# Optimization experiments

Hardware: AMD Instinct MI355X
Metric: run time of the kernel (lower is better)

Reference implementation:

```python
import jax, jax.numpy as jnp
import numpy as np

IN, OUT, HID = 64, 32, 256
B, T = 64, 256
NOISE_STD, TAU = 0.05, 0.2


def setup_inputs() -> dict:
    key = jax.random.key(0)
    ks = jax.random.split(key, 8)
    u = jax.random.normal(ks[0], (B, T, IN), dtype=jnp.float32)
    x0 = jax.random.normal(ks[1], (B, HID), dtype=jnp.float32)
    noise = jax.random.normal(ks[2], (T, B, HID), dtype=jnp.float32)
    w_hh_rnn = jax.random.normal(ks[3], (HID, HID), dtype=jnp.float32) * (0.1 / HID ** 0.5)
    w_hh_tbrnn = jax.random.normal(ks[4], (HID, HID, HID), dtype=jnp.float32) * (0.1 / HID)
    w_in_w = jax.random.normal(ks[5], (HID, IN), dtype=jnp.float32)
    w_in_b = jnp.zeros((HID,), dtype=jnp.float32)
    w_out_w = jax.random.normal(ks[6], (OUT, HID), dtype=jnp.float32) * 4.0
    w_out_b = jax.random.normal(ks[7], (OUT,), dtype=jnp.float32) * 0.0
    return {"u": u, "x0": x0, "noise": noise, "w_hh_rnn": w_hh_rnn,
            "w_hh_tbrnn": w_hh_tbrnn, "w_in_w": w_in_w, "w_in_b": w_in_b,
            "w_out_w": w_out_w, "w_out_b": w_out_b}


def reference(u, x0, noise, w_hh_rnn, w_hh_tbrnn, w_in_w, w_in_b, w_out_w, w_out_b):
    # mode='cont', form='rate', adv=False, nonlinearity=tanh, output_nonlinearity=tanh
    u_t_first = jnp.transpose(u, (1, 0, 2))  # [T, B, IN]

    def step(x, inp):
        u_t, n_t = inp
        r = jnp.tanh(x)                                   # rate form
        input_I = u_t @ w_in_w.T + w_in_b                 # [B, HID]
        hidden_W1 = r @ w_hh_rnn.T                        # [B, HID]
        # out[b,j] = sum_{i,k} r[b,i] * W[j,i,k] * r[b,k]
        hidden_W2 = jnp.einsum('bi,jik,bk->bj', r, w_hh_tbrnn, r)
        rec_x = hidden_W1 + hidden_W2 + input_I
        x_new = x + NOISE_STD * n_t + TAU * (-x + rec_x)  # cont mode
        return x_new, x_new

    x_final, traj = jax.lax.scan(step, x0, (u_t_first, noise))
    trajectories = jnp.transpose(traj, (1, 0, 2))         # [B, T, HID]
    output = jnp.tanh(trajectories) @ w_out_w.T + w_out_b  # [B, T, OUT]
    return output, x_final, trajectories
```

## Files before the change

### kernel.cpp

```cpp
#include <hip/hip_runtime.h>
#include <hip/hip_bf16.h>
#include <math.h>

#define HID 256
#define BSZ 64
#define TLEN 256
#define INW 64
#define OUTW 32
#define NOISE_STD 0.05f
#define TAU 0.2f

typedef __attribute__((ext_vector_type(8))) short short8;
typedef __attribute__((ext_vector_type(4))) short shortx4;
typedef __attribute__((ext_vector_type(4))) float floatx4;
typedef unsigned long long u64;

__device__ __forceinline__ int ridx(int b, int k) {
    int P = ((b >> 2) & 7) ^ ((b & 3) << 1);
    return b * 256 + ((((k >> 3) ^ P) & 31) << 3) + (k & 7);
}

__global__ __launch_bounds__(256) void swizzle_kernel(const float* __restrict__ W,
                                                      __hip_bfloat16* __restrict__ Wsw) {
    int g = blockIdx.x * 256 + threadIdx.x;
    int l  = g & 63;
    int ni = (g >> 6) & 15;
    int kk = (g >> 10) & 7;
    int j  = g >> 13;
    int i  = ni * 16 + (l & 15);
    int k0 = kk * 32 + (l >> 4) * 8;
    const float* __restrict__ src = W + ((size_t)j * HID + i) * HID + k0;
    __hip_bfloat16* __restrict__ dst = Wsw + (size_t)g * 8;
#pragma unroll
    for (int e = 0; e < 8; ++e) dst[e] = __float2bfloat16(src[e]);
}

__global__ __launch_bounds__(256) void init_kernel(const float* __restrict__ x0,
                                                   u64* __restrict__ buf0) {
    int g = blockIdx.x;
    int k = threadIdx.x;
    u64 v = 0;
#pragma unroll
    for (int e = 0; e < 4; ++e) {
        __hip_bfloat16 h = __float2bfloat16(tanhf(x0[(4 * g + e) * HID + k]));
        v |= (u64)(*(unsigned short*)&h) << (16 * e);
    }
    buf0[g * 256 + k] = v;
}

__global__ __launch_bounds__(256) void pre_kernel(const float* __restrict__ u,
                                                  const float* __restrict__ w_in_w,
                                                  const float* __restrict__ w_in_b,
                                                  const float* __restrict__ noise,
                                                  float* __restrict__ pre) {
    __shared__ float ulds[BSZ][INW + 4];
    const int t = blockIdx.x;
    const int j = threadIdx.x;
    {
        int b = threadIdx.x >> 2, q = threadIdx.x & 3;
#pragma unroll
        for (int e = 0; e < 4; ++e) {
            float4 v = *(const float4*)(u + ((size_t)b * TLEN + t) * INW + q * 16 + e * 4);
            *(float4*)&ulds[b][q * 16 + e * 4] = v;
        }
    }
    float wreg[INW];
#pragma unroll
    for (int q = 0; q < INW / 4; ++q) {
        float4 v = *(const float4*)(w_in_w + (size_t)j * INW + q * 4);
        wreg[q * 4 + 0] = v.x; wreg[q * 4 + 1] = v.y;
        wreg[q * 4 + 2] = v.z; wreg[q * 4 + 3] = v.w;
    }
    float bias = w_in_b[j];
    __syncthreads();
    for (int b = 0; b < BSZ; ++b) {
        float s = bias;
#pragma unroll
        for (int in_ = 0; in_ < INW; ++in_) s = fmaf(ulds[b][in_], wreg[in_], s);
        float nz = noise[((size_t)t * BSZ + b) * HID + j];
        pre[((size_t)t * HID + j) * BSZ + b] = NOISE_STD * nz + TAU * s;
    }
}

__global__ __launch_bounds__(256, 1) void persist_kernel(
    const __hip_bfloat16* __restrict__ Wsw,
    const float* __restrict__ w_hh,
    const float* __restrict__ u,
    const float* __restrict__ w_in_w,
    const float* __restrict__ w_in_b,
    const float* __restrict__ noise,
    const float* __restrict__ x0,
    u64* __restrict__ buf0,
    u64* __restrict__ buf1,
    float* __restrict__ traj,
    float* __restrict__ trajWS,
    float* __restrict__ xfinal,
    int* __restrict__ ready,
    const float* __restrict__ pre,
    int use_pre, int use_tws) {
    __shared__ short rlds[16384];
    __shared__ float redw[256];
    __shared__ char lds_pad[57344];

    const int tid  = threadIdx.x;
    const int j    = blockIdx.x;
    const int w    = tid >> 6;
    const int lane = tid & 63;
    const int quad = lane >> 4;
    const int col  = lane & 15;

    if (j == 0x7fffffff) lds_pad[tid] = 0;

    short8 wreg[32];
    {
        const short* __restrict__ wsh = (const short*)Wsw;
#pragma unroll
        for (int kk = 0; kk < 8; ++kk)
#pragma unroll
            for (int mt = 0; mt < 4; ++mt)
                wreg[kk * 4 + mt] = *(const short8*)(wsh +
                    ((((size_t)j * 8 + kk) * 16 + (w * 4 + mt)) * 64 + lane) * 8);
    }
    float whh16[16];
#pragma unroll
    for (int mt = 0; mt < 4; ++mt)
#pragma unroll
        for (int rg = 0; rg < 4; ++rg)
            whh16[mt * 4 + rg] = w_hh[j * HID + (w * 4 + mt) * 16 + quad * 4 + rg];

    float xb = 0.f;
    if (tid < BSZ) xb = x0[tid * HID + j];

#pragma unroll 1
    for (int t = 0; t < TLEN; ++t) {
        const u64* __restrict__ rcur = (t & 1) ? buf1 : buf0;
        u64* __restrict__ rnxt = (t & 1) ? buf0 : buf1;

        float extra = 0.f;
        if (tid < BSZ) {
            if (use_pre) {
                extra = pre[((size_t)t * HID + j) * BSZ + tid];
            } else {
                float isum = w_in_b[j];
                const float4* __restrict__ urow =
                    (const float4*)(u + ((size_t)tid * TLEN + t) * INW);
                const float4* __restrict__ wrow = (const float4*)(w_in_w + (size_t)j * INW);
#pragma unroll
                for (int q = 0; q < INW / 4; ++q) {
                    float4 uu = urow[q], ww = wrow[q];
                    isum = fmaf(uu.x, ww.x, isum);
                    isum = fmaf(uu.y, ww.y, isum);
                    isum = fmaf(uu.z, ww.z, isum);
                    isum = fmaf(uu.w, ww.w, isum);
                }
                float nz = noise[((size_t)t * BSZ + tid) * HID + j];
                extra = NOISE_STD * nz + TAU * isum;
            }
        }

        if (t > 0) {
            while (__hip_atomic_load(ready + tid * 16, __ATOMIC_RELAXED,
                                     __HIP_MEMORY_SCOPE_AGENT) < t)
                __builtin_amdgcn_s_sleep(1);
            asm volatile("" ::: "memory");
        }

        {
            u64 v[16];
#pragma unroll
            for (int g = 0; g < 16; ++g)
                v[g] = __hip_atomic_load(rcur + g * 256 + tid, __ATOMIC_RELAXED,
                                         __HIP_MEMORY_SCOPE_AGENT);
#pragma unroll
            for (int g = 0; g < 16; ++g)
#pragma unroll
                for (int e = 0; e < 4; ++e)
                    rlds[ridx(4 * g + e, tid)] = (short)(v[g] >> (16 * e));
        }
        __syncthreads();

        floatx4 acc[4][4];
#pragma unroll
        for (int mt = 0; mt < 4; ++mt)
#pragma unroll
            for (int nt = 0; nt < 4; ++nt) acc[mt][nt] = (floatx4){0.f, 0.f, 0.f, 0.f};

#pragma unroll
        for (int kk = 0; kk < 8; ++kk) {
            short8 afrag[4];
#pragma unroll
            for (int nt = 0; nt < 4; ++nt)
                afrag[nt] = *(const short8*)&rlds[ridx(nt * 16 + col, kk * 32 + quad * 8)];
#pragma unroll
            for (int mt = 0; mt < 4; ++mt)
#pragma unroll
                for (int nt = 0; nt < 4; ++nt)
                    acc[mt][nt] = __builtin_amdgcn_mfma_f32_16x16x32_bf16(
                        wreg[kk * 4 + mt], afrag[nt], acc[mt][nt], 0, 0, 0);
        }

        float part[4];
#pragma unroll
        for (int nt = 0; nt < 4; ++nt) part[nt] = 0.f;
#pragma unroll
        for (int mt = 0; mt < 4; ++mt) {
            const int ib = (w * 4 + mt) * 16 + quad * 4;
#pragma unroll
            for (int nt = 0; nt < 4; ++nt) {
                const int b = nt * 16 + col;
                shortx4 r4 = *(const shortx4*)&rlds[ridx(b, ib)];
#pragma unroll
                for (int rg = 0; rg < 4; ++rg) {
                    short rs = r4[rg];
                    float rv = __bfloat162float(*(__hip_bfloat16*)&rs);
                    part[nt] = fmaf(rv, acc[mt][nt][rg] + whh16[mt * 4 + rg], part[nt]);
                }
            }
        }
#pragma unroll
        for (int nt = 0; nt < 4; ++nt) {
            part[nt] += __shfl_xor(part[nt], 16, 64);
            part[nt] += __shfl_xor(part[nt], 32, 64);
        }
        if (quad == 0) {
#pragma unroll
            for (int nt = 0; nt < 4; ++nt)
                redw[w * 64 + nt * 16 + col] = part[nt];
        }
        __syncthreads();

        if (w == 0) {
            const int b = lane;
            float rec = redw[b] + redw[64 + b] + redw[128 + b] + redw[192 + b];
            float xn = xb + extra + TAU * (rec - xb);
            xb = xn;

            if (t < TLEN - 1) {
                __hip_bfloat16 h = __float2bfloat16(tanhf(xn));
                int hs = (int)(*(unsigned short*)&h);
                int src = 4 * (lane & 15);
                u64 pv = (u64)(unsigned)__shfl(hs, src + 0, 64)
                       | ((u64)(unsigned)__shfl(hs, src + 1, 64) << 16)
                       | ((u64)(unsigned)__shfl(hs, src + 2, 64) << 32)
                       | ((u64)(unsigned)__shfl(hs, src + 3, 64) << 48);
                if (lane < 16)
                    __hip_atomic_store(rnxt + (size_t)lane * 256 + j, pv,
                                       __ATOMIC_RELAXED, __HIP_MEMORY_SCOPE_AGENT);
                asm volatile("s_waitcnt vmcnt(0)" ::: "memory");
                if (lane == 0)
                    __hip_atomic_store(ready + j * 16, t + 1, __ATOMIC_RELAXED,
                                       __HIP_MEMORY_SCOPE_AGENT);
            }

            if (use_tws) {
                trajWS[((size_t)t * HID + j) * BSZ + b] = xn;
            } else {
                traj[((size_t)b * TLEN + t) * HID + j] = xn;
                if (t == TLEN - 1) xfinal[b * HID + j] = xn;
            }
        }
    }
}

__global__ __launch_bounds__(256) void fixup_kernel(
    const float* __restrict__ trajWS,
    const float* __restrict__ w_out_w,
    const float* __restrict__ w_out_b,
    float* __restrict__ traj,
    float* __restrict__ xfinal,
    float* __restrict__ out) {
    __shared__ float xv[BSZ * 257];
    __shared__ float wol[OUTW * 257];
    const int t = blockIdx.x, tid = threadIdx.x;

#pragma unroll
    for (int it = 0; it < 16; ++it) {
        int flat = it * 1024 + tid * 4;
        float4 v = *(const float4*)(trajWS + (size_t)t * 16384 + flat);
        int jj = flat >> 6, b = flat & 63;
        xv[(b + 0) * 257 + jj] = v.x;
        xv[(b + 1) * 257 + jj] = v.y;
        xv[(b + 2) * 257 + jj] = v.z;
        xv[(b + 3) * 257 + jj] = v.w;
    }
#pragma unroll
    for (int it = 0; it < 8; ++it) {
        int flat = it * 1024 + tid * 4;
        float4 v = *(const float4*)(w_out_w + flat);
        int o = flat >> 8, h = flat & 255;
        *(float4*)&wol[o * 257 + h] = v;
    }
    __syncthreads();

    for (int b = 0; b < BSZ; ++b)
        traj[((size_t)b * TLEN + t) * HID + tid] = xv[b * 257 + tid];
    if (t == TLEN - 1)
        for (int b = 0; b < BSZ; ++b)
            xfinal[b * HID + tid] = xv[b * 257 + tid];

    __syncthreads();
#pragma unroll
    for (int it = 0; it < 64; ++it)
        xv[it * 257 + tid] = tanhf(xv[it * 257 + tid]);
    __syncthreads();

    const int o = tid & 31;
    const float bias = w_out_b[o];
#pragma unroll 1
    for (int rep = 0; rep < 8; ++rep) {
        int b = rep * 8 + (tid >> 5);
        float s = bias;
#pragma unroll 8
        for (int h = 0; h < HID; ++h)
            s = fmaf(xv[b * 257 + h], wol[o * 257 + h], s);
        out[((size_t)b * TLEN + t) * OUTW + o] = s;
    }
}

__global__ __launch_bounds__(256) void output_kernel(
    const float* __restrict__ traj, const float* __restrict__ w_out_w,
    const float* __restrict__ w_out_b, float* __restrict__ out) {
    __shared__ float th[8][HID + 1];
    const int bt0 = blockIdx.x * 8;
    const int tid = threadIdx.x;
#pragma unroll
    for (int m = 0; m < 8; ++m) {
        int idx = m * 256 + tid;
        th[idx >> 8][idx & 255] = tanhf(traj[(size_t)bt0 * HID + idx]);
    }
    __syncthreads();
    const int row = tid >> 5, o = tid & 31;
    const float* __restrict__ wrow = w_out_w + (size_t)o * HID;
    float s = w_out_b[o];
#pragma unroll 8
    for (int h = 0; h < HID; ++h) s = fmaf(th[row][h], wrow[h], s);
    out[(size_t)(bt0 + row) * OUTW + o] = s;
}

extern "C" void kernel_launch(void* const* d_in, const int* in_sizes, int n_in,
                              void* d_out, int out_size, void* d_ws, size_t ws_size,
                              hipStream_t stream) {
    const float* u       = (const float*)d_in[0];
    const float* x0      = (const float*)d_in[1];
    const float* noise   = (const float*)d_in[2];
    const float* w_hh    = (const float*)d_in[3];
    const float* W       = (const float*)d_in[4];
    const float* w_in_w  = (const float*)d_in[5];
    const float* w_in_b  = (const float*)d_in[6];
    const float* w_out_w = (const float*)d_in[7];
    const float* w_out_b = (const float*)d_in[8];

    float* out    = (float*)d_out;
    float* xfinal = out + (size_t)BSZ * TLEN * OUTW;
    float* traj   = xfinal + (size_t)BSZ * HID;

    char* ws = (char*)d_ws;
    __hip_bfloat16* Wsw = (__hip_bfloat16*)ws;
    u64*   buf0 = (u64*)(ws + 33554432);
    u64*   buf1 = (u64*)(ws + 33587200);
    int*   rdy  = (int*)(ws + 33619968);
    float* tws  = (float*)(ws + 33636352);
    float* pre  = (float*)(ws + 50413568);
    const size_t NEED_TWS = 50413568ull;
    const size_t NEED_PRE = 67190784ull;
    const int use_tws = (ws_size >= NEED_TWS) ? 1 : 0;
    const int use_pre = (ws_size >= NEED_PRE) ? 1 : 0;

    hipMemsetAsync(rdy, 0, 16384, stream);
    swizzle_kernel<<<8192, 256, 0, stream>>>(W, Wsw);
    init_kernel<<<16, 256, 0, stream>>>(x0, buf0);
    if (use_pre)
        pre_kernel<<<TLEN, 256, 0, stream>>>(u, w_in_w, w_in_b, noise, pre);

    persist_kernel<<<256, 256, 0, stream>>>(
        Wsw, w_hh, u, w_in_w, w_in_b, noise, x0,
        buf0, buf1, traj, tws, xfinal, rdy, pre, use_pre, use_tws);

    if (use_tws)
        fixup_kernel<<<TLEN, 256, 0, stream>>>(tws, w_out_w, w_out_b, traj, xfinal, out);
    else
        output_kernel<<<(BSZ * TLEN) / 8, 256, 0, stream>>>(traj, w_out_w, w_out_b, out);
}
```

Measured before the change: 1.471 ms.

## Split K across two wave groups in persistent recurrent kernel with 512 threads

```diff
diff --git a/kernel.cpp b/kernel.cpp
--- a/kernel.cpp
+++ b/kernel.cpp
@@ -82,7 +82,7 @@
     }
 }
 
-__global__ __launch_bounds__(256, 1) void persist_kernel(
+__global__ __launch_bounds__(512, 1) void persist_kernel(
     const __hip_bfloat16* __restrict__ Wsw,
     const float* __restrict__ w_hh,
     const float* __restrict__ u,
@@ -99,8 +99,7 @@
     const float* __restrict__ pre,
     int use_pre, int use_tws) {
     __shared__ short rlds[16384];
-    __shared__ float redw[256];
-    __shared__ char lds_pad[57344];
+    __shared__ float redw[512];
 
     const int tid  = threadIdx.x;
     const int j    = blockIdx.x;
@@ -108,25 +107,28 @@
     const int lane = tid & 63;
     const int quad = lane >> 4;
     const int col  = lane & 15;
-
-    if (j == 0x7fffffff) lds_pad[tid] = 0;
-
-    short8 wreg[32];
+    const int wk   = w >> 2;
+    const int wi   = w & 3;
+    const int kcol = tid & 255;
+    const int gb   = (tid >> 8) * 8;
+
+    short8 wreg[16];
     {
         const short* __restrict__ wsh = (const short*)Wsw;
 #pragma unroll
-        for (int kk = 0; kk < 8; ++kk)
+        for (int kkl = 0; kkl < 4; ++kkl)
 #pragma unroll
             for (int mt = 0; mt < 4; ++mt)
-                wreg[kk * 4 + mt] = *(const short8*)(wsh +
-                    ((((size_t)j * 8 + kk) * 16 + (w * 4 + mt)) * 64 + lane) * 8);
+                wreg[kkl * 4 + mt] = *(const short8*)(wsh +
+                    ((((size_t)j * 8 + (wk * 4 + kkl)) * 16 + (wi * 4 + mt)) * 64 + lane) * 8);
     }
     float whh16[16];
 #pragma unroll
     for (int mt = 0; mt < 4; ++mt)
 #pragma unroll
         for (int rg = 0; rg < 4; ++rg)
-            whh16[mt * 4 + rg] = w_hh[j * HID + (w * 4 + mt) * 16 + quad * 4 + rg];
+            whh16[mt * 4 + rg] = (wk == 0)
+                ? w_hh[j * HID + (wi * 4 + mt) * 16 + quad * 4 + rg] : 0.f;
 
     float xb = 0.f;
     if (tid < BSZ) xb = x0[tid * HID + j];
@@ -159,23 +161,23 @@
         }
 
         if (t > 0) {
-            while (__hip_atomic_load(ready + tid * 16, __ATOMIC_RELAXED,
+            while (__hip_atomic_load(ready + kcol * 16, __ATOMIC_RELAXED,
                                      __HIP_MEMORY_SCOPE_AGENT) < t)
                 __builtin_amdgcn_s_sleep(1);
             asm volatile("" ::: "memory");
         }
 
         {
-            u64 v[16];
-#pragma unroll
-            for (int g = 0; g < 16; ++g)
-                v[g] = __hip_atomic_load(rcur + g * 256 + tid, __ATOMIC_RELAXED,
-                                         __HIP_MEMORY_SCOPE_AGENT);
-#pragma unroll
-            for (int g = 0; g < 16; ++g)
+            u64 v[8];
+#pragma unroll
+            for (int gg = 0; gg < 8; ++gg)
+                v[gg] = __hip_atomic_load(rcur + (gb + gg) * 256 + kcol,
+                                          __ATOMIC_RELAXED, __HIP_MEMORY_SCOPE_AGENT);
+#pragma unroll
+            for (int gg = 0; gg < 8; ++gg)
 #pragma unroll
                 for (int e = 0; e < 4; ++e)
-                    rlds[ridx(4 * g + e, tid)] = (short)(v[g] >> (16 * e));
+                    rlds[ridx(4 * (gb + gg) + e, kcol)] = (short)(v[gg] >> (16 * e));
         }
         __syncthreads();
 
@@ -183,20 +185,23 @@
 #pragma unroll
         for (int mt = 0; mt < 4; ++mt)
 #pragma unroll
-            for (int nt = 0; nt < 4; ++nt) acc[mt][nt] = (floatx4){0.f, 0.f, 0.f, 0.f};
-
-#pragma unroll
-        for (int kk = 0; kk < 8; ++kk) {
+            for (int nt = 0; nt < 4; ++nt)
+                acc[mt][nt] = (floatx4){whh16[mt * 4 + 0], whh16[mt * 4 + 1],
+                                        whh16[mt * 4 + 2], whh16[mt * 4 + 3]};
+
+#pragma unroll
+        for (int kkl = 0; kkl < 4; ++kkl) {
             short8 afrag[4];
 #pragma unroll
             for (int nt = 0; nt < 4; ++nt)
-                afrag[nt] = *(const short8*)&rlds[ridx(nt * 16 + col, kk * 32 + quad * 8)];
+                afrag[nt] = *(const short8*)&rlds[
+                    ridx(nt * 16 + col, (wk * 4 + kkl) * 32 + quad * 8)];
 #pragma unroll
             for (int mt = 0; mt < 4; ++mt)
 #pragma unroll
                 for (int nt = 0; nt < 4; ++nt)
                     acc[mt][nt] = __builtin_amdgcn_mfma_f32_16x16x32_bf16(
-                        wreg[kk * 4 + mt], afrag[nt], acc[mt][nt], 0, 0, 0);
+                        wreg[kkl * 4 + mt], afrag[nt], acc[mt][nt], 0, 0, 0);
         }
 
         float part[4];
@@ -204,7 +209,7 @@
         for (int nt = 0; nt < 4; ++nt) part[nt] = 0.f;
 #pragma unroll
         for (int mt = 0; mt < 4; ++mt) {
-            const int ib = (w * 4 + mt) * 16 + quad * 4;
+            const int ib = (wi * 4 + mt) * 16 + quad * 4;
 #pragma unroll
             for (int nt = 0; nt < 4; ++nt) {
                 const int b = nt * 16 + col;
@@ -213,7 +218,7 @@
                 for (int rg = 0; rg < 4; ++rg) {
                     short rs = r4[rg];
                     float rv = __bfloat162float(*(__hip_bfloat16*)&rs);
-                    part[nt] = fmaf(rv, acc[mt][nt][rg] + whh16[mt * 4 + rg], part[nt]);
+                    part[nt] = fmaf(rv, acc[mt][nt][rg], part[nt]);
                 }
             }
         }
@@ -231,7 +236,9 @@
 
         if (w == 0) {
             const int b = lane;
-            float rec = redw[b] + redw[64 + b] + redw[128 + b] + redw[192 + b];
+            float rec = 0.f;
+#pragma unroll
+            for (int s = 0; s < 8; ++s) rec += redw[s * 64 + b];
             float xn = xb + extra + TAU * (rec - xb);
             xb = xn;
 
@@ -372,7 +379,7 @@
     if (use_pre)
         pre_kernel<<<TLEN, 256, 0, stream>>>(u, w_in_w, w_in_b, noise, pre);
 
-    persist_kernel<<<256, 256, 0, stream>>>(
+    persist_kernel<<<256, 512, 0, stream>>>(
         Wsw, w_hh, u, w_in_w, w_in_b, noise, x0,
         buf0, buf1, traj, tws, xfinal, rdy, pre, use_pre, use_tws);
 
```

After: 1.971 ms. +34.0%, slower.

## Replace double buffer with sentinel-marked triple ring to overlap state loads with flag wait

Applied to the files above, without the earlier changes.

```diff
diff --git a/kernel.cpp b/kernel.cpp
--- a/kernel.cpp
+++ b/kernel.cpp
@@ -9,6 +9,7 @@
 #define OUTW 32
 #define NOISE_STD 0.05f
 #define TAU 0.2f
+#define SENT 0xFFFFFFFFFFFFFFFFull
 
 typedef __attribute__((ext_vector_type(8))) short short8;
 typedef __attribute__((ext_vector_type(4))) short shortx4;
@@ -36,7 +37,7 @@
 }
 
 __global__ __launch_bounds__(256) void init_kernel(const float* __restrict__ x0,
-                                                   u64* __restrict__ buf0) {
+                                                   u64* __restrict__ ring0) {
     int g = blockIdx.x;
     int k = threadIdx.x;
     u64 v = 0;
@@ -45,7 +46,7 @@
         __hip_bfloat16 h = __float2bfloat16(tanhf(x0[(4 * g + e) * HID + k]));
         v |= (u64)(*(unsigned short*)&h) << (16 * e);
     }
-    buf0[g * 256 + k] = v;
+    ring0[g * 256 + k] = v;
 }
 
 __global__ __launch_bounds__(256) void pre_kernel(const float* __restrict__ u,
@@ -90,8 +91,7 @@
     const float* __restrict__ w_in_b,
     const float* __restrict__ noise,
     const float* __restrict__ x0,
-    u64* __restrict__ buf0,
-    u64* __restrict__ buf1,
+    u64* __restrict__ ring,
     float* __restrict__ traj,
     float* __restrict__ trajWS,
     float* __restrict__ xfinal,
@@ -133,8 +133,14 @@
 
 #pragma unroll 1
     for (int t = 0; t < TLEN; ++t) {
-        const u64* __restrict__ rcur = (t & 1) ? buf1 : buf0;
-        u64* __restrict__ rnxt = (t & 1) ? buf0 : buf1;
+        const u64* __restrict__ rslot = ring + (size_t)(t % 3) * 4096;
+        u64* __restrict__ wslot = ring + (size_t)((t + 1) % 3) * 4096;
+
+        u64 v[16];
+#pragma unroll
+        for (int g = 0; g < 16; ++g)
+            v[g] = __hip_atomic_load(rslot + g * 256 + tid, __ATOMIC_RELAXED,
+                                     __HIP_MEMORY_SCOPE_AGENT);
 
         float extra = 0.f;
         if (tid < BSZ) {
@@ -163,27 +169,38 @@
                                      __HIP_MEMORY_SCOPE_AGENT) < t)
                 __builtin_amdgcn_s_sleep(1);
             asm volatile("" ::: "memory");
-        }
-
-        {
-            u64 v[16];
-#pragma unroll
-            for (int g = 0; g < 16; ++g)
-                v[g] = __hip_atomic_load(rcur + g * 256 + tid, __ATOMIC_RELAXED,
-                                         __HIP_MEMORY_SCOPE_AGENT);
-#pragma unroll
-            for (int g = 0; g < 16; ++g)
-#pragma unroll
-                for (int e = 0; e < 4; ++e)
-                    rlds[ridx(4 * g + e, tid)] = (short)(v[g] >> (16 * e));
-        }
+            int pend = 1;
+            while (pend) {
+                pend = 0;
+#pragma unroll
+                for (int g = 0; g < 16; ++g)
+                    if (v[g] == SENT) {
+                        v[g] = __hip_atomic_load(rslot + g * 256 + tid,
+                                                 __ATOMIC_RELAXED,
+                                                 __HIP_MEMORY_SCOPE_AGENT);
+                        pend |= (v[g] == SENT);
+                    }
+            }
+        }
+
+#pragma unroll
+        for (int g = 0; g < 16; ++g)
+#pragma unroll
+            for (int e = 0; e < 4; ++e)
+                rlds[ridx(4 * g + e, tid)] = (short)(v[g] >> (16 * e));
         __syncthreads();
 
+        if (w == 0 && lane < 16)
+            __hip_atomic_store(ring + (size_t)((t + 2) % 3) * 4096 + lane * 256 + j,
+                               SENT, __ATOMIC_RELAXED, __HIP_MEMORY_SCOPE_AGENT);
+
         floatx4 acc[4][4];
 #pragma unroll
         for (int mt = 0; mt < 4; ++mt)
 #pragma unroll
-            for (int nt = 0; nt < 4; ++nt) acc[mt][nt] = (floatx4){0.f, 0.f, 0.f, 0.f};
+            for (int nt = 0; nt < 4; ++nt)
+                acc[mt][nt] = (floatx4){whh16[mt * 4 + 0], whh16[mt * 4 + 1],
+                                        whh16[mt * 4 + 2], whh16[mt * 4 + 3]};
 
 #pragma unroll
         for (int kk = 0; kk < 8; ++kk) {
@@ -213,7 +230,7 @@
                 for (int rg = 0; rg < 4; ++rg) {
                     short rs = r4[rg];
                     float rv = __bfloat162float(*(__hip_bfloat16*)&rs);
-                    part[nt] = fmaf(rv, acc[mt][nt][rg] + whh16[mt * 4 + rg], part[nt]);
+                    part[nt] = fmaf(rv, acc[mt][nt][rg], part[nt]);
                 }
             }
         }
@@ -244,7 +261,7 @@
                        | ((u64)(unsigned)__shfl(hs, src + 2, 64) << 32)
                        | ((u64)(unsigned)__shfl(hs, src + 3, 64) << 48);
                 if (lane < 16)
-                    __hip_atomic_store(rnxt + (size_t)lane * 256 + j, pv,
+                    __hip_atomic_store(wslot + (size_t)lane * 256 + j, pv,
                                        __ATOMIC_RELAXED, __HIP_MEMORY_SCOPE_AGENT);
                 asm volatile("s_waitcnt vmcnt(0)" ::: "memory");
                 if (lane == 0)
@@ -356,25 +373,25 @@
 
     char* ws = (char*)d_ws;
     __hip_bfloat16* Wsw = (__hip_bfloat16*)ws;
-    u64*   buf0 = (u64*)(ws + 33554432);
-    u64*   buf1 = (u64*)(ws + 33587200);
-    int*   rdy  = (int*)(ws + 33619968);
-    float* tws  = (float*)(ws + 33636352);
-    float* pre  = (float*)(ws + 50413568);
-    const size_t NEED_TWS = 50413568ull;
-    const size_t NEED_PRE = 67190784ull;
+    u64*   ring = (u64*)(ws + 33554432);
+    int*   rdy  = (int*)(ws + 33652736);
+    float* tws  = (float*)(ws + 33669120);
+    float* pre  = (float*)(ws + 50446336);
+    const size_t NEED_TWS = 50446336ull;
+    const size_t NEED_PRE = 67223552ull;
     const int use_tws = (ws_size >= NEED_TWS) ? 1 : 0;
     const int use_pre = (ws_size >= NEED_PRE) ? 1 : 0;
 
     hipMemsetAsync(rdy, 0, 16384, stream);
+    hipMemsetAsync((char*)ring + 32768, 0xFF, 65536, stream);
     swizzle_kernel<<<8192, 256, 0, stream>>>(W, Wsw);
-    init_kernel<<<16, 256, 0, stream>>>(x0, buf0);
+    init_kernel<<<16, 256, 0, stream>>>(x0, ring);
     if (use_pre)
         pre_kernel<<<TLEN, 256, 0, stream>>>(u, w_in_w, w_in_b, noise, pre);
 
     persist_kernel<<<256, 256, 0, stream>>>(
         Wsw, w_hh, u, w_in_w, w_in_b, noise, x0,
-        buf0, buf1, traj, tws, xfinal, rdy, pre, use_pre, use_tws);
+        ring, traj, tws, xfinal, rdy, pre, use_pre, use_tws);
 
     if (use_tws)
         fixup_kernel<<<TLEN, 256, 0, stream>>>(tws, w_out_w, w_out_b, traj, xfinal, out);
```

Result: slower. 3.120 ms (+112.0%).

## Split recurrent state fetch into halves and overlap second half with MFMA

Applied to the files above, without the earlier changes.

```diff
diff --git a/kernel.cpp b/kernel.cpp
--- a/kernel.cpp
+++ b/kernel.cpp
@@ -100,7 +100,6 @@
     int use_pre, int use_tws) {
     __shared__ short rlds[16384];
     __shared__ float redw[256];
-    __shared__ char lds_pad[57344];
 
     const int tid  = threadIdx.x;
     const int j    = blockIdx.x;
@@ -108,8 +107,9 @@
     const int lane = tid & 63;
     const int quad = lane >> 4;
     const int col  = lane & 15;
-
-    if (j == 0x7fffffff) lds_pad[tid] = 0;
+    const int kL   = tid & 127;
+    const int kH   = kL + 128;
+    const int gb   = (tid >> 7) * 8;
 
     short8 wreg[32];
     {
@@ -159,23 +159,22 @@
         }
 
         if (t > 0) {
-            while (__hip_atomic_load(ready + tid * 16, __ATOMIC_RELAXED,
+            while (__hip_atomic_load(ready + kL * 16, __ATOMIC_RELAXED,
                                      __HIP_MEMORY_SCOPE_AGENT) < t)
                 __builtin_amdgcn_s_sleep(1);
             asm volatile("" ::: "memory");
         }
-
         {
-            u64 v[16];
-#pragma unroll
-            for (int g = 0; g < 16; ++g)
-                v[g] = __hip_atomic_load(rcur + g * 256 + tid, __ATOMIC_RELAXED,
-                                         __HIP_MEMORY_SCOPE_AGENT);
-#pragma unroll
-            for (int g = 0; g < 16; ++g)
+            u64 vl[8];
+#pragma unroll
+            for (int gg = 0; gg < 8; ++gg)
+                vl[gg] = __hip_atomic_load(rcur + (gb + gg) * 256 + kL,
+                                           __ATOMIC_RELAXED, __HIP_MEMORY_SCOPE_AGENT);
+#pragma unroll
+            for (int gg = 0; gg < 8; ++gg)
 #pragma unroll
                 for (int e = 0; e < 4; ++e)
-                    rlds[ridx(4 * g + e, tid)] = (short)(v[g] >> (16 * e));
+                    rlds[ridx(4 * (gb + gg) + e, kL)] = (short)(vl[gg] >> (16 * e));
         }
         __syncthreads();
 
@@ -183,10 +182,17 @@
 #pragma unroll
         for (int mt = 0; mt < 4; ++mt)
 #pragma unroll
-            for (int nt = 0; nt < 4; ++nt) acc[mt][nt] = (floatx4){0.f, 0.f, 0.f, 0.f};
-
-#pragma unroll
-        for (int kk = 0; kk < 8; ++kk) {
+            for (int nt = 0; nt < 4; ++nt)
+                acc[mt][nt] = (floatx4){whh16[mt * 4 + 0], whh16[mt * 4 + 1],
+                                        whh16[mt * 4 + 2], whh16[mt * 4 + 3]};
+
+        int fh = t;
+        if (t > 0)
+            fh = __hip_atomic_load(ready + kH * 16, __ATOMIC_RELAXED,
+                                   __HIP_MEMORY_SCOPE_AGENT);
+
+#pragma unroll
+        for (int kk = 0; kk < 2; ++kk) {
             short8 afrag[4];
 #pragma unroll
             for (int nt = 0; nt < 4; ++nt)
@@ -199,6 +205,55 @@
                         wreg[kk * 4 + mt], afrag[nt], acc[mt][nt], 0, 0, 0);
         }
 
+        if (t > 0 && fh < t) {
+            do {
+                __builtin_amdgcn_s_sleep(1);
+                fh = __hip_atomic_load(ready + kH * 16, __ATOMIC_RELAXED,
+                                       __HIP_MEMORY_SCOPE_AGENT);
+            } while (fh < t);
+        }
+        asm volatile("" ::: "memory");
+        u64 vh[8];
+#pragma unroll
+        for (int gg = 0; gg < 8; ++gg)
+            vh[gg] = __hip_atomic_load(rcur + (gb + gg) * 256 + kH,
+                                       __ATOMIC_RELAXED, __HIP_MEMORY_SCOPE_AGENT);
+
+#pragma unroll
+        for (int kk = 2; kk < 4; ++kk) {
+            short8 afrag[4];
+#pragma unroll
+            for (int nt = 0; nt < 4; ++nt)
+                afrag[nt] = *(const short8*)&rlds[ridx(nt * 16 + col, kk * 32 + quad * 8)];
+#pragma unroll
+            for (int mt = 0; mt < 4; ++mt)
+#pragma unroll
+                for (int nt = 0; nt < 4; ++nt)
+                    acc[mt][nt] = __builtin_amdgcn_mfma_f32_16x16x32_bf16(
+                        wreg[kk * 4 + mt], afrag[nt], acc[mt][nt], 0, 0, 0);
+        }
+
+#pragma unroll
+        for (int gg = 0; gg < 8; ++gg)
+#pragma unroll
+            for (int e = 0; e < 4; ++e)
+                rlds[ridx(4 * (gb + gg) + e, kH)] = (short)(vh[gg] >> (16 * e));
+        __syncthreads();
+
+#pragma unroll
+        for (int kk = 4; kk < 8; ++kk) {
+            short8 afrag[4];
+#pragma unroll
+            for (int nt = 0; nt < 4; ++nt)
+                afrag[nt] = *(const short8*)&rlds[ridx(nt * 16 + col, kk * 32 + quad * 8)];
+#pragma unroll
+            for (int mt = 0; mt < 4; ++mt)
+#pragma unroll
+                for (int nt = 0; nt < 4; ++nt)
+                    acc[mt][nt] = __builtin_amdgcn_mfma_f32_16x16x32_bf16(
+                        wreg[kk * 4 + mt], afrag[nt], acc[mt][nt], 0, 0, 0);
+        }
+
         float part[4];
 #pragma unroll
         for (int nt = 0; nt < 4; ++nt) part[nt] = 0.f;
@@ -213,7 +268,7 @@
                 for (int rg = 0; rg < 4; ++rg) {
                     short rs = r4[rg];
                     float rv = __bfloat162float(*(__hip_bfloat16*)&rs);
-                    part[nt] = fmaf(rv, acc[mt][nt][rg] + whh16[mt * 4 + rg], part[nt]);
+                    part[nt] = fmaf(rv, acc[mt][nt][rg], part[nt]);
                 }
             }
         }
```

Measured after the change: 1.529 ms. 3.9% more time.
